# Performance work log

Hardware: AMD Instinct MI355X
Metric: run time of the kernel (lower is better)

The kernel has to match this reference:

```python
import jax, jax.numpy as jnp
import numpy as np

# --- constants matching DILConfig ---
N_DIFF = 1000      # num_diffusion_steps
STEPS = 4          # inference_steps
S_MAX = 4          # max_scales
BUDGET = 0.2       # entropy_budget
G0 = 2.0           # guidance_strength
ENT_LO = 0.1       # stability_threshold_low
ENT_HI = 0.5       # stability_threshold_high
B, L, C, H = 16, 1024, 128, 512


def setup_inputs() -> dict:
    key = jax.random.key(0)
    ks = jax.random.split(key, 6)
    y_obs = jax.random.normal(ks[0], (B, L, C), dtype=jnp.float32)
    mask = (jax.random.uniform(ks[1], (B, L, C)) > 0.5).astype(jnp.float32)
    z_init = jax.random.normal(ks[2], (B, L, C), dtype=jnp.float32)
    W1 = jax.random.normal(ks[3], (C, H), dtype=jnp.float32) / np.sqrt(C)
    b1 = jnp.zeros((H,), dtype=jnp.float32)
    W2 = jax.random.normal(ks[4], (H, C), dtype=jnp.float32) / np.sqrt(H)
    b2 = jnp.zeros((C,), dtype=jnp.float32)
    tw = jax.random.normal(ks[5], (H,), dtype=jnp.float32)
    return {"y_obs": y_obs, "mask": mask, "z_init": z_init,
            "W1": W1, "b1": b1, "W2": W2, "b2": b2, "tw": tw}


def _dil_forward(y_obs, mask, z_init, W1, b1, W2, b2, tw):
    # diffusion schedule (linear betas)
    betas = jnp.linspace(1e-4, 0.02, N_DIFF, dtype=jnp.float32)
    ac = jnp.cumprod(1.0 - betas)
    alpha = jnp.sqrt(ac)                     # sqrt_alphas_cumprod
    sigma = jnp.sqrt(1.0 - ac)               # sqrt_one_minus_alphas_cumprod
    lam = jnp.log(alpha) - jnp.log(sigma)    # log-SNR/2

    step = N_DIFF // STEPS
    ks = [N_DIFF - 1 - i * step for i in range(STEPS)]

    def score(z, k):
        # epsilon predictor: channel MLP with scalar time feature
        t_feat = jnp.float32(k) / N_DIFF
        h = jax.nn.gelu(jnp.einsum('blc,ch->blh', z, W1) + b1 + t_feat * tw)
        return jnp.einsum('blh,hc->blc', h, W2) + b2

    z = z_init
    for k in ks:  # fixed small unrolled loop over inference steps
        kp = max(k - step, 0)
        eps = score(z, k)                                   # [B,L,C]
        h_lam = lam[kp] - lam[k]
        base_a = alpha[kp] / alpha[k]
        base_b = sigma[kp] * (jnp.exp(h_lam) - 1.0)

        # entropy map: batch-mean |eps| per pixel
        ent_pix = jnp.mean(jnp.abs(eps), axis=0)            # [L,C]

        # self-guidance on observed entries
        obs_err = (z - y_obs) * mask
        guidance = -obs_err / (jnp.var(obs_err) + 1e-8)     # [B,L,C]

        z_new = z
        # coarse -> fine so finer-scale selected nodes overwrite coarser ones
        for s in range(S_MAX - 1, -1, -1):
            w = 2 ** s
            pooled = ent_pix.reshape(L // w, w, C // w, w).mean(axis=(1, 3))
            Knodes = max(1, int(BUDGET * pooled.size))
            _, idx = jax.lax.top_k(pooled.ravel(), Knodes)
            selg = jnp.zeros((pooled.size,), jnp.float32).at[idx].set(1.0)
            selg = selg.reshape(pooled.shape)
            sel = jnp.repeat(jnp.repeat(selg, w, axis=0), w, axis=1)     # [L,C]
            ent_up = jnp.repeat(jnp.repeat(pooled, w, axis=0), w, axis=1)

            # adaptive solver order from entropy stability thresholds
            order = (1.0 + (ent_up > ENT_LO).astype(jnp.float32)
                         + (ent_up > ENT_HI).astype(jnp.float32))
            corr = (1.0 + (order - 1.0) * 0.5 * h_lam
                        + (order - 1.0) * (order - 2.0) / 6.0 * h_lam ** 2)
            gs = G0 * ent_up / (ent_up + 1.0)               # adaptive guidance

            cand = base_a * z - base_b * (corr * eps) + gs * guidance
            z_new = jnp.where(sel[None, :, :] > 0, cand, z_new)
        z = z_new
    return z


def reference(y_obs, mask, z_init, W1, b1, W2, b2, tw):
    return _dil_forward(y_obs, mask, z_init, W1, b1, W2, b2, tw)
```

## Files before the change

kernel.cpp:

```cpp
#include <hip/hip_runtime.h>
#include <math.h>
#include <stdint.h>

#define L_DIM 1024
#define C_DIM 128
#define H_DIM 512
#define B_DIM 16
#define LC (L_DIM * C_DIM)
#define BLC (B_DIM * LC)

typedef __attribute__((ext_vector_type(8))) short short8;
typedef __attribute__((ext_vector_type(4))) float floatx4;

__device__ __forceinline__ unsigned fordbits(unsigned u) {
    return (u & 0x80000000u) ? ~u : (u | 0x80000000u);
}

__device__ __forceinline__ void split3(float x, unsigned& uh, unsigned& um,
                                       unsigned& ul) {
    uh = __float_as_uint(x);
    const float r1 = x - __uint_as_float(uh & 0xffff0000u);
    um = __float_as_uint(r1);
    const float r2 = r1 - __uint_as_float(um & 0xffff0000u);
    ul = __float_as_uint(r2);
}

__device__ __forceinline__ float gelu_fast(float x) {
    const float g = 0.7978845608028654f * (x + 0.044715f * x * x * x);
    const float e = __expf(2.0f * g);
    const float t = 1.0f - 2.0f / (e + 1.0f);
    return 0.5f * x * (1.0f + t);
}

__global__ __launch_bounds__(256) void wsplit_kernel(
    const float* __restrict__ W1, const float* __restrict__ W2,
    unsigned short* __restrict__ W1h, unsigned short* __restrict__ W1m,
    unsigned short* __restrict__ W1l, unsigned short* __restrict__ W2h,
    unsigned short* __restrict__ W2m, unsigned short* __restrict__ W2l,
    unsigned* __restrict__ zeroblk) {
    const int t = blockIdx.x * 256 + threadIdx.x;
    if (t < 16396) zeroblk[t] = 0u;
    unsigned uh, um, ul;
    if (t < 65536) {
        const int j = t & 7, lane = (t >> 3) & 63, nt = (t >> 9) & 31,
                  kt = (t >> 14) & 3;
        const int k = kt * 32 + (lane >> 4) * 8 + j;
        const int n = nt * 16 + (lane & 15);
        split3(W1[k * 512 + n], uh, um, ul);
        W1h[t] = (unsigned short)(uh >> 16);
        W1m[t] = (unsigned short)(um >> 16);
        W1l[t] = (unsigned short)(ul >> 16);
    } else {
        const int t2 = t - 65536;
        const int j = t2 & 7, lane = (t2 >> 3) & 63, nt = (t2 >> 9) & 7,
                  kt = (t2 >> 12) & 15;
        const int k = kt * 32 + (lane >> 4) * 8 + j;
        const int n = nt * 16 + (lane & 15);
        split3(W2[k * 128 + n], uh, um, ul);
        W2h[t2] = (unsigned short)(uh >> 16);
        W2m[t2] = (unsigned short)(um >> 16);
        W2l[t2] = (unsigned short)(ul >> 16);
    }
}

#define MFMA6(AH, AM, AL, BH, BM, BL, ACC)                                    \
    ACC = __builtin_amdgcn_mfma_f32_16x16x32_bf16(AL, BH, ACC, 0, 0, 0);      \
    ACC = __builtin_amdgcn_mfma_f32_16x16x32_bf16(AM, BM, ACC, 0, 0, 0);      \
    ACC = __builtin_amdgcn_mfma_f32_16x16x32_bf16(AH, BL, ACC, 0, 0, 0);      \
    ACC = __builtin_amdgcn_mfma_f32_16x16x32_bf16(AM, BH, ACC, 0, 0, 0);      \
    ACC = __builtin_amdgcn_mfma_f32_16x16x32_bf16(AH, BM, ACC, 0, 0, 0);      \
    ACC = __builtin_amdgcn_mfma_f32_16x16x32_bf16(AH, BH, ACC, 0, 0, 0);

__device__ __forceinline__ int swz(int row, int col) {
    return row * 128 + ((((col >> 3) ^ (row & 15))) << 3) + (col & 7);
}

template <int UPD>
__global__ __launch_bounds__(512, 2) void mlp_kernel(
    float* __restrict__ z, const float* __restrict__ zr,
    const float* __restrict__ y, const float* __restrict__ mk,
    const unsigned short* __restrict__ W1h, const unsigned short* __restrict__ W1m,
    const unsigned short* __restrict__ W1l, const unsigned short* __restrict__ W2h,
    const unsigned short* __restrict__ W2m, const unsigned short* __restrict__ W2l,
    const float* __restrict__ b1, const float* __restrict__ tw,
    const float* __restrict__ b2, float t_feat,
    float* __restrict__ eps_buf, float* __restrict__ ent,
    const float* __restrict__ cA, const float* __restrict__ cB,
    const float* __restrict__ cG, float* __restrict__ accum) {
    __shared__ unsigned short zA[3][8192];
    __shared__ unsigned short hA[3][8192];
    __shared__ float red1[8], red2[8];
    const int tid = threadIdx.x;
    const int w = tid >> 6, lane = tid & 63;
    const int quad = lane >> 4, m16 = lane & 15;
    const int l0 = blockIdx.x * 4;

    float s1 = 0.f, s2 = 0.f;
#pragma unroll
    for (int e = 0; e < 4; ++e) {
        const int f = (e * 512 + tid) * 4;
        const int r_ = f >> 7, cb = f & 127;
        const int b = r_ & 15, il = r_ >> 4, l = l0 + il;
        const size_t g = ((size_t)b * 1024 + l) * 128 + cb;
        float4 zv = *(const float4*)(zr + g);
        const float4 yv = *(const float4*)(y + g);
        const float4 mv = *(const float4*)(mk + g);
        if (UPD) {
            const float4 ev = *(const float4*)(eps_buf + g);
            const int pix = l * 128 + cb;
            const float4 a4 = *(const float4*)(cA + pix);
            const float4 b4 = *(const float4*)(cB + pix);
            const float4 g4 = *(const float4*)(cG + pix);
            zv.x = a4.x * zv.x - b4.x * ev.x - g4.x * ((zv.x - yv.x) * mv.x);
            zv.y = a4.y * zv.y - b4.y * ev.y - g4.y * ((zv.y - yv.y) * mv.y);
            zv.z = a4.z * zv.z - b4.z * ev.z - g4.z * ((zv.z - yv.z) * mv.z);
            zv.w = a4.w * zv.w - b4.w * ev.w - g4.w * ((zv.w - yv.w) * mv.w);
            *(float4*)(z + g) = zv;
        }
        float oe;
        oe = (zv.x - yv.x) * mv.x; s1 += oe; s2 += oe * oe;
        oe = (zv.y - yv.y) * mv.y; s1 += oe; s2 += oe * oe;
        oe = (zv.z - yv.z) * mv.z; s1 += oe; s2 += oe * oe;
        oe = (zv.w - yv.w) * mv.w; s1 += oe; s2 += oe * oe;

        const int base = swz(r_, cb);
        const float xs[4] = {zv.x, zv.y, zv.z, zv.w};
        ushort4 vh, vm, vl;
        unsigned uh, um, ul;
        split3(xs[0], uh, um, ul); vh.x = uh >> 16; vm.x = um >> 16; vl.x = ul >> 16;
        split3(xs[1], uh, um, ul); vh.y = uh >> 16; vm.y = um >> 16; vl.y = ul >> 16;
        split3(xs[2], uh, um, ul); vh.z = uh >> 16; vm.z = um >> 16; vl.z = ul >> 16;
        split3(xs[3], uh, um, ul); vh.w = uh >> 16; vm.w = um >> 16; vl.w = ul >> 16;
        *(ushort4*)(&zA[0][base]) = vh;
        *(ushort4*)(&zA[1][base]) = vm;
        *(ushort4*)(&zA[2][base]) = vl;
    }
#pragma unroll
    for (int off = 32; off; off >>= 1) {
        s1 += __shfl_down(s1, off);
        s2 += __shfl_down(s2, off);
    }
    if (lane == 0) { red1[w] = s1; red2[w] = s2; }
    __syncthreads();
    if (tid == 0) {
        float a1 = 0.f, a2 = 0.f;
#pragma unroll
        for (int i = 0; i < 8; ++i) { a1 += red1[i]; a2 += red2[i]; }
        atomicAdd(&accum[0], a1);
        atomicAdd(&accum[1], a2);
    }

    floatx4 acc1[16];
#pragma unroll
    for (int i = 0; i < 16; ++i) acc1[i] = (floatx4){0.f, 0.f, 0.f, 0.f};

#pragma unroll
    for (int kt = 0; kt < 4; ++kt) {
        short8 Ah[4], Am[4], Al[4];
#pragma unroll
        for (int il = 0; il < 4; ++il) {
            const int fb = swz(il * 16 + m16, kt * 32 + quad * 8);
            Ah[il] = *(const short8*)(&zA[0][fb]);
            Am[il] = *(const short8*)(&zA[1][fb]);
            Al[il] = *(const short8*)(&zA[2][fb]);
        }
#pragma unroll
        for (int q = 0; q < 4; ++q) {
            const size_t off = ((size_t)(kt * 32 + q * 8 + w) * 64 + lane) * 8;
            const short8 bh = *(const short8*)(W1h + off);
            const short8 bm = *(const short8*)(W1m + off);
            const short8 bl = *(const short8*)(W1l + off);
#pragma unroll
            for (int il = 0; il < 4; ++il) {
                floatx4 a = acc1[q * 4 + il];
                MFMA6(Ah[il], Am[il], Al[il], bh, bm, bl, a);
                acc1[q * 4 + il] = a;
            }
        }
    }

    floatx4 acc2[4];
#pragma unroll
    for (int i = 0; i < 4; ++i) acc2[i] = (floatx4){0.f, 0.f, 0.f, 0.f};

#pragma unroll
    for (int q = 0; q < 4; ++q) {
        {
            const int colg = q * 128 + w * 16 + m16;
            const float bb = b1[colg] + t_feat * tw[colg];
            const int kcol = w * 16 + m16;
#pragma unroll
            for (int il = 0; il < 4; ++il) {
#pragma unroll
                for (int r = 0; r < 4; ++r) {
                    const float x = gelu_fast(acc1[q * 4 + il][r] + bb);
                    unsigned uh, um, ul;
                    split3(x, uh, um, ul);
                    const int idx = swz(il * 16 + quad * 4 + r, kcol);
                    hA[0][idx] = (unsigned short)(uh >> 16);
                    hA[1][idx] = (unsigned short)(um >> 16);
                    hA[2][idx] = (unsigned short)(ul >> 16);
                }
            }
        }
        __syncthreads();

#pragma unroll
        for (int ktl = 0; ktl < 4; ++ktl) {
            short8 Ah2[4], Am2[4], Al2[4];
#pragma unroll
            for (int il = 0; il < 4; ++il) {
                const int fb = swz(il * 16 + m16, ktl * 32 + quad * 8);
                Ah2[il] = *(const short8*)(&hA[0][fb]);
                Am2[il] = *(const short8*)(&hA[1][fb]);
                Al2[il] = *(const short8*)(&hA[2][fb]);
            }
            const size_t off =
                ((size_t)((q * 4 + ktl) * 8 + w) * 64 + lane) * 8;
            const short8 bh = *(const short8*)(W2h + off);
            const short8 bm = *(const short8*)(W2m + off);
            const short8 bl = *(const short8*)(W2l + off);
#pragma unroll
            for (int il = 0; il < 4; ++il) {
                floatx4 a = acc2[il];
                MFMA6(Ah2[il], Am2[il], Al2[il], bh, bm, bl, a);
                acc2[il] = a;
            }
        }
        __syncthreads();
    }

    {
        const int col = w * 16 + m16;
        const float bb2 = b2[col];
#pragma unroll
        for (int il = 0; il < 4; ++il) {
            float pa = 0.f;
#pragma unroll
            for (int r = 0; r < 4; ++r) {
                const float e = acc2[il][r] + bb2;
                const int b = quad * 4 + r;
                eps_buf[((size_t)b * 1024 + l0 + il) * 128 + col] = e;
                pa += fabsf(e);
            }
            pa += __shfl_xor(pa, 16);
            pa += __shfl_xor(pa, 32);
            if (quad == 0) ent[(l0 + il) * 128 + col] = pa * (1.0f / 16.0f);
        }
    }
}


__global__ __launch_bounds__(256) void pools_kernel(
    const float* __restrict__ ent, float* __restrict__ p1,
    float* __restrict__ p2, float* __restrict__ p3,
    unsigned* __restrict__ ghist) {
    __shared__ unsigned lh[8192];
    const int tid = threadIdx.x;
    const int gid = blockIdx.x * 256 + tid;
    for (int i = tid; i < 8192; i += 256) lh[i] = 0u;
    __syncthreads();

    {
        const float2 ev = *(const float2*)(ent + (size_t)gid * 2);
        const unsigned b0 = fordbits(__float_as_uint(ev.x)) >> 18;
        const unsigned b1_ = fordbits(__float_as_uint(ev.y)) >> 18;
        atomicAdd(&lh[b0 >> 1], 1u << ((b0 & 1) << 4));
        atomicAdd(&lh[b1_ >> 1], 1u << ((b1_ & 1) << 4));
    }
    if (gid < 32768) {
        const int r = gid >> 6, c = gid & 63;
        float s = 0.f;
#pragma unroll
        for (int ii = 0; ii < 2; ++ii) {
            const float2 e = *(const float2*)(ent + (((r * 2 + ii) << 7) + c * 2));
            s += e.x; s += e.y;
        }
        p1[gid] = s * 0.25f;
    }
    if (gid < 8192) {
        const int r = gid >> 5, c = gid & 31;
        float s = 0.f;
#pragma unroll
        for (int ii = 0; ii < 4; ++ii) {
            const float4 e = *(const float4*)(ent + (((r * 4 + ii) << 7) + c * 4));
            s += e.x; s += e.y; s += e.z; s += e.w;
        }
        p2[gid] = s * 0.0625f;
    }
    if (gid < 2048) {
        const int r = gid >> 4, c = gid & 15;
        float s = 0.f;
#pragma unroll
        for (int ii = 0; ii < 8; ++ii) {
            const float4 ea = *(const float4*)(ent + (((r * 8 + ii) << 7) + c * 8));
            const float4 eb = *(const float4*)(ent + (((r * 8 + ii) << 7) + c * 8 + 4));
            s += ea.x; s += ea.y; s += ea.z; s += ea.w;
            s += eb.x; s += eb.y; s += eb.z; s += eb.w;
        }
        p3[gid] = s * (1.0f / 64.0f);
    }
    __syncthreads();
    for (int i = tid; i < 8192; i += 256) {
        const unsigned v = lh[i];
        if (v & 0xFFFFu) atomicAdd(&ghist[2 * i], v & 0xFFFFu);
        if (v >> 16) atomicAdd(&ghist[2 * i + 1], v >> 16);
    }
}

#define CAND_CAP 16384

template <int NPT4, int N, unsigned K>
__device__ __forceinline__ void small_select(
    const float* __restrict__ data, unsigned* __restrict__ gout, const int t,
    const int w8, unsigned* __restrict__ histcand,
    unsigned* __restrict__ part, unsigned (*hrep)[512],
    unsigned* sh_b, unsigned* sh_krem, unsigned* sh_cnt, unsigned* sh_d,
    unsigned* sh_k2) {
    float4 xv[NPT4];
#pragma unroll
    for (int i = 0; i < NPT4; ++i) {
        const int idx4 = t + i * 1024;
        if (idx4 < (N >> 2)) xv[i] = ((const float4*)data)[idx4];
        else xv[i] = (float4){-1e30f, -1e30f, -1e30f, -1e30f};
    }
    unsigned u[NPT4 * 4];
#pragma unroll
    for (int i = 0; i < NPT4; ++i) {
        u[4 * i + 0] = fordbits(__float_as_uint(xv[i].x));
        u[4 * i + 1] = fordbits(__float_as_uint(xv[i].y));
        u[4 * i + 2] = fordbits(__float_as_uint(xv[i].z));
        u[4 * i + 3] = fordbits(__float_as_uint(xv[i].w));
    }
    if (t == 0) { *sh_b = 0u; *sh_krem = 1u; *sh_cnt = 0u; *sh_d = 0u; *sh_k2 = 1u; }
    for (int i = t; i < 16384; i += 1024) histcand[i] = 0u;
    __syncthreads();
#pragma unroll
    for (int j = 0; j < NPT4 * 4; ++j) atomicAdd(&histcand[u[j] >> 18], 1u);
    __syncthreads();
    {
        unsigned s = 0;
#pragma unroll
        for (int j = 0; j < 16; ++j) s += histcand[t * 16 + j];
        part[t] = s;
    }
    __syncthreads();
    for (int off = 1; off < 1024; off <<= 1) {
        const unsigned v = (t + off < 1024) ? part[t + off] : 0u;
        __syncthreads();
        part[t] += v;
        __syncthreads();
    }
    {
        const unsigned suf = part[t];
        const unsigned sufn = (t < 1023) ? part[t + 1] : 0u;
        if (suf >= K && sufn < K) {
            unsigned run = sufn;
            for (int b = 15; b >= 0; --b) {
                const unsigned hb = histcand[t * 16 + b];
                run += hb;
                if (run >= K) {
                    *sh_b = (unsigned)(t * 16 + b);
                    *sh_krem = K - (run - hb);
                    break;
                }
            }
        }
    }
    __syncthreads();
    const unsigned b14 = *sh_b;
    unsigned krem = *sh_krem;
    __syncthreads();
#pragma unroll
    for (int j = 0; j < NPT4 * 4; ++j)
        if ((u[j] >> 18) == b14) {
            const unsigned p = atomicAdd(sh_cnt, 1u);
            if (p < CAND_CAP) histcand[p] = u[j];
        }
    __syncthreads();
    const unsigned cnt = *sh_cnt;
    const bool inlds = (cnt <= CAND_CAP);
    for (int i = t; i < 4096; i += 1024) ((unsigned*)hrep)[i] = 0u;
    __syncthreads();
    if (inlds) {
        for (unsigned i = t; i < cnt; i += 1024)
            atomicAdd(&hrep[w8][(histcand[i] >> 9) & 511u], 1u);
    } else {
#pragma unroll
        for (int j = 0; j < NPT4 * 4; ++j)
            if ((u[j] >> 18) == b14)
                atomicAdd(&hrep[w8][(u[j] >> 9) & 511u], 1u);
    }
    __syncthreads();
    if (t < 512) {
        unsigned s = 0;
#pragma unroll
        for (int r = 0; r < 8; ++r) s += hrep[r][t];
        part[t] = s;
    }
    __syncthreads();
    for (int off = 1; off < 512; off <<= 1) {
        unsigned v = 0u;
        if (t < 512) v = (t + off < 512) ? part[t + off] : 0u;
        __syncthreads();
        if (t < 512) part[t] += v;
        __syncthreads();
    }
    if (t < 512) {
        const unsigned suf = part[t];
        const unsigned sufn = (t < 511) ? part[t + 1] : 0u;
        if (suf >= krem && sufn < krem) { *sh_d = (unsigned)t; *sh_k2 = krem - sufn; }
    }
    __syncthreads();
    const unsigned dA = *sh_d;
    krem = *sh_k2;
    __syncthreads();
    for (int i = t; i < 4096; i += 1024) ((unsigned*)hrep)[i] = 0u;
    __syncthreads();
    if (inlds) {
        for (unsigned i = t; i < cnt; i += 1024) {
            const unsigned c = histcand[i];
            if (((c >> 9) & 511u) == dA) atomicAdd(&hrep[w8][c & 511u], 1u);
        }
    } else {
#pragma unroll
        for (int j = 0; j < NPT4 * 4; ++j)
            if ((u[j] >> 18) == b14 && ((u[j] >> 9) & 511u) == dA)
                atomicAdd(&hrep[w8][u[j] & 511u], 1u);
    }
    __syncthreads();
    if (t < 512) {
        unsigned s = 0;
#pragma unroll
        for (int r = 0; r < 8; ++r) s += hrep[r][t];
        part[t] = s;
    }
    __syncthreads();
    for (int off = 1; off < 512; off <<= 1) {
        unsigned v = 0u;
        if (t < 512) v = (t + off < 512) ? part[t + off] : 0u;
        __syncthreads();
        if (t < 512) part[t] += v;
        __syncthreads();
    }
    if (t < 512) {
        const unsigned suf = part[t];
        const unsigned sufn = (t < 511) ? part[t + 1] : 0u;
        if (suf >= krem && sufn < krem)
            gout[0] = (b14 << 18) | (dA << 9) | (unsigned)t;
    }
}

__global__ __launch_bounds__(1024, 1) void thresh_kernel(
    const float* __restrict__ ent, const float* __restrict__ p1,
    const float* __restrict__ p2, const float* __restrict__ p3,
    const unsigned* __restrict__ ghist, unsigned* __restrict__ gprefix) {
    const int scale = blockIdx.x, t = threadIdx.x;
    __shared__ unsigned histcand[16384];
    __shared__ unsigned part[1024];
    __shared__ unsigned hrep[8][512];
    __shared__ unsigned sh_b, sh_krem, sh_cnt, sh_d, sh_k2;
    const int w8 = (t >> 6) & 7;

    if (scale == 1) {
        small_select<8, 32768, 6553u>(p1, &gprefix[1], t, w8, histcand, part,
                                      hrep, &sh_b, &sh_krem, &sh_cnt, &sh_d,
                                      &sh_k2);
        return;
    }
    if (scale == 2) {
        small_select<2, 8192, 1638u>(p2, &gprefix[2], t, w8, histcand, part,
                                     hrep, &sh_b, &sh_krem, &sh_cnt, &sh_d,
                                     &sh_k2);
        return;
    }
    if (scale == 3) {
        small_select<1, 2048, 409u>(p3, &gprefix[3], t, w8, histcand, part,
                                    hrep, &sh_b, &sh_krem, &sh_cnt, &sh_d,
                                    &sh_k2);
        return;
    }

    const unsigned K = 26214u;
    if (t == 0) { sh_b = 0u; sh_krem = 1u; sh_cnt = 0u; sh_d = 0u; sh_k2 = 1u; }

    {
        unsigned s = 0;
        const uint4* h4 = (const uint4*)(ghist + t * 16);
#pragma unroll
        for (int j = 0; j < 4; ++j) {
            const uint4 x = h4[j];
            s += x.x + x.y + x.z + x.w;
        }
        part[t] = s;
    }
    __syncthreads();
    for (int off = 1; off < 1024; off <<= 1) {
        const unsigned v = (t + off < 1024) ? part[t + off] : 0u;
        __syncthreads();
        part[t] += v;
        __syncthreads();
    }
    {
        const unsigned suf = part[t];
        const unsigned sufn = (t < 1023) ? part[t + 1] : 0u;
        if (suf >= K && sufn < K) {
            unsigned run = sufn;
            for (int b = 15; b >= 0; --b) {
                const unsigned hb = ghist[t * 16 + b];
                run += hb;
                if (run >= K) {
                    sh_b = (unsigned)(t * 16 + b);
                    sh_krem = K - (run - hb);
                    break;
                }
            }
        }
    }
    __syncthreads();
    const unsigned b14 = sh_b;
    unsigned krem = sh_krem;

    for (int base = 0; base < 32768; base += 8192) {
        float4 w4[8];
#pragma unroll
        for (int i = 0; i < 8; ++i)
            w4[i] = ((const float4*)ent)[base + i * 1024 + t];
#pragma unroll
        for (int i = 0; i < 8; ++i) {
            const float xs[4] = {w4[i].x, w4[i].y, w4[i].z, w4[i].w};
#pragma unroll
            for (int j = 0; j < 4; ++j) {
                const unsigned uu = fordbits(__float_as_uint(xs[j]));
                if ((uu >> 18) == b14) {
                    const unsigned p = atomicAdd(&sh_cnt, 1u);
                    if (p < CAND_CAP) histcand[p] = uu;
                }
            }
        }
    }
    __syncthreads();
    const unsigned cnt = sh_cnt;
    const bool inlds = (cnt <= CAND_CAP);

    for (int i = t; i < 4096; i += 1024) ((unsigned*)hrep)[i] = 0u;
    __syncthreads();
    if (inlds) {
        for (unsigned i = t; i < cnt; i += 1024)
            atomicAdd(&hrep[w8][(histcand[i] >> 9) & 511u], 1u);
    } else {
        for (int base = 0; base < 32768; base += 8192) {
            float4 w4[8];
#pragma unroll
            for (int i = 0; i < 8; ++i)
                w4[i] = ((const float4*)ent)[base + i * 1024 + t];
#pragma unroll
            for (int i = 0; i < 8; ++i) {
                const float xs[4] = {w4[i].x, w4[i].y, w4[i].z, w4[i].w};
#pragma unroll
                for (int j = 0; j < 4; ++j) {
                    const unsigned uu = fordbits(__float_as_uint(xs[j]));
                    if ((uu >> 18) == b14)
                        atomicAdd(&hrep[w8][(uu >> 9) & 511u], 1u);
                }
            }
        }
    }
    __syncthreads();
    if (t < 512) {
        unsigned s = 0;
#pragma unroll
        for (int r = 0; r < 8; ++r) s += hrep[r][t];
        part[t] = s;
    }
    __syncthreads();
    for (int off = 1; off < 512; off <<= 1) {
        unsigned v = 0u;
        if (t < 512) v = (t + off < 512) ? part[t + off] : 0u;
        __syncthreads();
        if (t < 512) part[t] += v;
        __syncthreads();
    }
    if (t < 512) {
        const unsigned suf = part[t];
        const unsigned sufn = (t < 511) ? part[t + 1] : 0u;
        if (suf >= krem && sufn < krem) { sh_d = (unsigned)t; sh_k2 = krem - sufn; }
    }
    __syncthreads();
    const unsigned dA = sh_d;
    krem = sh_k2;
    __syncthreads();

    for (int i = t; i < 4096; i += 1024) ((unsigned*)hrep)[i] = 0u;
    __syncthreads();
    if (inlds) {
        for (unsigned i = t; i < cnt; i += 1024) {
            const unsigned c = histcand[i];
            if (((c >> 9) & 511u) == dA) atomicAdd(&hrep[w8][c & 511u], 1u);
        }
    } else {
        for (int base = 0; base < 32768; base += 8192) {
            float4 w4[8];
#pragma unroll
            for (int i = 0; i < 8; ++i)
                w4[i] = ((const float4*)ent)[base + i * 1024 + t];
#pragma unroll
            for (int i = 0; i < 8; ++i) {
                const float xs[4] = {w4[i].x, w4[i].y, w4[i].z, w4[i].w};
#pragma unroll
                for (int j = 0; j < 4; ++j) {
                    const unsigned uu = fordbits(__float_as_uint(xs[j]));
                    if ((uu >> 18) == b14 && ((uu >> 9) & 511u) == dA)
                        atomicAdd(&hrep[w8][uu & 511u], 1u);
                }
            }
        }
    }
    __syncthreads();
    if (t < 512) {
        unsigned s = 0;
#pragma unroll
        for (int r = 0; r < 8; ++r) s += hrep[r][t];
        part[t] = s;
    }
    __syncthreads();
    for (int off = 1; off < 512; off <<= 1) {
        unsigned v = 0u;
        if (t < 512) v = (t + off < 512) ? part[t + off] : 0u;
        __syncthreads();
        if (t < 512) part[t] += v;
        __syncthreads();
    }
    if (t < 512) {
        const unsigned suf = part[t];
        const unsigned sufn = (t < 511) ? part[t + 1] : 0u;
        if (suf >= krem && sufn < krem)
            gprefix[0] = (b14 << 18) | (dA << 9) | (unsigned)t;
    }
}

__global__ __launch_bounds__(256) void coeff_kernel(
    const float* __restrict__ ent, const float* __restrict__ p1,
    const float* __restrict__ p2, const float* __restrict__ p3,
    const unsigned* __restrict__ gprefix, const float* __restrict__ accum_si,
    float* __restrict__ cA, float* __restrict__ cB, float* __restrict__ cG,
    unsigned* __restrict__ ghist, float base_a, float base_b, float h_lam) {
    const int i = blockIdx.x * 256 + threadIdx.x;
    if (i < 16384) ghist[i] = 0u;

    const unsigned t0 = gprefix[0], t1 = gprefix[1], t2 = gprefix[2],
                   t3 = gprefix[3];
    const float mean = accum_si[0] * (1.0f / (float)BLC);
    const float var = accum_si[1] * (1.0f / (float)BLC) - mean * mean;
    const float vinv = 1.0f / (var + 1e-8f);

    const int l = i >> 7, c = i & 127;
    float ent_v = 0.f;
    bool sel = false;
    const float v0 = ent[i];
    if (fordbits(__float_as_uint(v0)) >= t0) { ent_v = v0; sel = true; }
    else {
        const float v1 = p1[((l >> 1) << 6) + (c >> 1)];
        if (fordbits(__float_as_uint(v1)) >= t1) { ent_v = v1; sel = true; }
        else {
            const float v2 = p2[((l >> 2) << 5) + (c >> 2)];
            if (fordbits(__float_as_uint(v2)) >= t2) { ent_v = v2; sel = true; }
            else {
                const float v3 = p3[((l >> 3) << 4) + (c >> 3)];
                if (fordbits(__float_as_uint(v3)) >= t3) { ent_v = v3; sel = true; }
            }
        }
    }
    if (sel) {
        float corr;
        if (ent_v > 0.5f)
            corr = 1.0f + h_lam + h_lam * h_lam * (1.0f / 3.0f);
        else if (ent_v > 0.1f)
            corr = 1.0f + 0.5f * h_lam;
        else
            corr = 1.0f;
        cA[i] = base_a;
        cB[i] = base_b * corr;
        cG[i] = (2.0f * ent_v / (ent_v + 1.0f)) * vinv;
    } else {
        cA[i] = 1.0f;
        cB[i] = 0.f;
        cG[i] = 0.f;
    }
}

__global__ __launch_bounds__(256) void update_kernel(
    float* __restrict__ z, const float* __restrict__ y,
    const float* __restrict__ mk, const float* __restrict__ eps,
    const float* __restrict__ cA, const float* __restrict__ cB,
    const float* __restrict__ cG) {
    const int idx = blockIdx.x * 256 + threadIdx.x;
    const int p = idx & (LC - 1);
    const float zi = z[idx];
    z[idx] = cA[p] * zi - cB[p] * eps[idx] - cG[p] * ((zi - y[idx]) * mk[idx]);
}

extern "C" void kernel_launch(void* const* d_in, const int* in_sizes, int n_in,
                              void* d_out, int out_size, void* d_ws,
                              size_t ws_size, hipStream_t stream) {
    const float* y_obs = (const float*)d_in[0];
    const float* mask = (const float*)d_in[1];
    const float* z_init = (const float*)d_in[2];
    const float* W1 = (const float*)d_in[3];
    const float* b1 = (const float*)d_in[4];
    const float* W2 = (const float*)d_in[5];
    const float* b2 = (const float*)d_in[6];
    const float* tw = (const float*)d_in[7];
    float* z = (float*)d_out;
    float* ws = (float*)d_ws;

    float* eps = ws;
    float* ent = ws + 2097152;
    float* p1 = ws + 2228224;
    float* p2 = ws + 2260992;
    float* p3 = ws + 2269184;
    float* cA = ws + 2271232;
    float* cB = ws + 2402304;
    float* cG = ws + 2533376;
    float* accum = ws + 2664448;
    unsigned* gprefix = (unsigned*)(ws + 2664456);
    unsigned* ghist = (unsigned*)(ws + 2664460);
    unsigned short* W1h = (unsigned short*)(ws + 2680844);
    unsigned short* W1m = (unsigned short*)(ws + 2713612);
    unsigned short* W1l = (unsigned short*)(ws + 2746380);
    unsigned short* W2h = (unsigned short*)(ws + 2779148);
    unsigned short* W2m = (unsigned short*)(ws + 2811916);
    unsigned short* W2l = (unsigned short*)(ws + 2844684);

    float alpha_[1000], sigma_[1000], lam_[1000];
    {
        float ac = 1.0f;
        for (int i = 0; i < 1000; ++i) {
            const float beta = 1e-4f + (0.02f - 1e-4f) * ((float)i / 999.0f);
            ac = ac * (1.0f - beta);
            alpha_[i] = sqrtf(ac);
            sigma_[i] = sqrtf(1.0f - ac);
            lam_[i] = logf(alpha_[i]) - logf(sigma_[i]);
        }
    }
    float tf[4], hl[4], ba[4], bb[4];
    for (int si = 0; si < 4; ++si) {
        const int k = 999 - si * 250;
        const int kp = (k - 250 > 0) ? (k - 250) : 0;
        tf[si] = (float)k / 1000.0f;
        hl[si] = lam_[kp] - lam_[k];
        ba[si] = alpha_[kp] / alpha_[k];
        bb[si] = sigma_[kp] * (expf(hl[si]) - 1.0f);
    }

    wsplit_kernel<<<512, 256, 0, stream>>>(W1, W2, W1h, W1m, W1l, W2h, W2m,
                                           W2l, (unsigned*)accum);

    for (int si = 0; si < 4; ++si) {
        const float* zrd = (si <= 1) ? z_init : z;
        if (si == 0) {
            mlp_kernel<0><<<256, 512, 0, stream>>>(
                z, zrd, y_obs, mask, W1h, W1m, W1l, W2h, W2m, W2l, b1, tw, b2,
                tf[0], eps, ent, cA, cB, cG, accum);
        } else {
            mlp_kernel<1><<<256, 512, 0, stream>>>(
                z, zrd, y_obs, mask, W1h, W1m, W1l, W2h, W2m, W2l, b1, tw, b2,
                tf[si], eps, ent, cA, cB, cG, accum + 2 * si);
        }
        pools_kernel<<<256, 256, 0, stream>>>(ent, p1, p2, p3, ghist);
        thresh_kernel<<<4, 1024, 0, stream>>>(ent, p1, p2, p3, ghist, gprefix);
        coeff_kernel<<<512, 256, 0, stream>>>(ent, p1, p2, p3, gprefix,
                                              accum + 2 * si, cA, cB, cG,
                                              ghist, ba[si], bb[si], hl[si]);
    }
    update_kernel<<<8192, 256, 0, stream>>>(z, y_obs, mask, eps, cA, cB, cG);
}
```

Before: 384.2 us.

## Fuse entropy pooling and histogram into MLP kernel and prefetch weight fragments

Removes the separate pools_kernel by computing the 2x2 and 4x4 pooled entropy and the global radix histogram inside the MLP kernel's epilogue, reusing the hA shared buffer for the local histogram. The 8x8 pooling moves into the scale-3 block of thresh_kernel. It also software-pipelines the W1/W2 bf16 fragment loads by prefetching the next fragment before the current MFMAs. This saves one launch per step and a re-read of the entropy map, at the cost of more registers and a longer serial tail in the MLP kernel.

Result: faster. 370.5 us (median of 2 runs) (-3.6%).

```diff
diff --git a/kernel.cpp b/kernel.cpp
--- a/kernel.cpp
+++ b/kernel.cpp
@@ -86,9 +86,12 @@
     const float* __restrict__ b2, float t_feat,
     float* __restrict__ eps_buf, float* __restrict__ ent,
     const float* __restrict__ cA, const float* __restrict__ cB,
-    const float* __restrict__ cG, float* __restrict__ accum) {
+    const float* __restrict__ cG, float* __restrict__ accum,
+    float* __restrict__ p1, float* __restrict__ p2,
+    unsigned* __restrict__ ghist) {
     __shared__ unsigned short zA[3][8192];
     __shared__ unsigned short hA[3][8192];
+    __shared__ float entbuf[4][128];
     __shared__ float red1[8], red2[8];
     const int tid = threadIdx.x;
     const int w = tid >> 6, lane = tid & 63;
@@ -154,28 +157,43 @@
 #pragma unroll
     for (int i = 0; i < 16; ++i) acc1[i] = (floatx4){0.f, 0.f, 0.f, 0.f};
 
-#pragma unroll
-    for (int kt = 0; kt < 4; ++kt) {
+    {
         short8 Ah[4], Am[4], Al[4];
-#pragma unroll
-        for (int il = 0; il < 4; ++il) {
-            const int fb = swz(il * 16 + m16, kt * 32 + quad * 8);
-            Ah[il] = *(const short8*)(&zA[0][fb]);
-            Am[il] = *(const short8*)(&zA[1][fb]);
-            Al[il] = *(const short8*)(&zA[2][fb]);
-        }
-#pragma unroll
-        for (int q = 0; q < 4; ++q) {
-            const size_t off = ((size_t)(kt * 32 + q * 8 + w) * 64 + lane) * 8;
-            const short8 bh = *(const short8*)(W1h + off);
-            const short8 bm = *(const short8*)(W1m + off);
-            const short8 bl = *(const short8*)(W1l + off);
+        short8 bh, bm, bl;
+        {
+            const size_t off0 = ((size_t)w * 64 + lane) * 8;
+            bh = *(const short8*)(W1h + off0);
+            bm = *(const short8*)(W1m + off0);
+            bl = *(const short8*)(W1l + off0);
+        }
+#pragma unroll
+        for (int it = 0; it < 16; ++it) {
+            const int kt = it >> 2, q = it & 3;
+            if (q == 0) {
+#pragma unroll
+                for (int il = 0; il < 4; ++il) {
+                    const int fb = swz(il * 16 + m16, kt * 32 + quad * 8);
+                    Ah[il] = *(const short8*)(&zA[0][fb]);
+                    Am[il] = *(const short8*)(&zA[1][fb]);
+                    Al[il] = *(const short8*)(&zA[2][fb]);
+                }
+            }
+            short8 nbh = bh, nbm = bm, nbl = bl;
+            if (it < 15) {
+                const int itn = it + 1;
+                const size_t off =
+                    ((size_t)((itn >> 2) * 32 + (itn & 3) * 8 + w) * 64 + lane) * 8;
+                nbh = *(const short8*)(W1h + off);
+                nbm = *(const short8*)(W1m + off);
+                nbl = *(const short8*)(W1l + off);
+            }
 #pragma unroll
             for (int il = 0; il < 4; ++il) {
                 floatx4 a = acc1[q * 4 + il];
                 MFMA6(Ah[il], Am[il], Al[il], bh, bm, bl, a);
                 acc1[q * 4 + il] = a;
             }
+            bh = nbh; bm = nbm; bl = nbl;
         }
     }
 
@@ -183,6 +201,13 @@
 #pragma unroll
     for (int i = 0; i < 4; ++i) acc2[i] = (floatx4){0.f, 0.f, 0.f, 0.f};
 
+    short8 ch, cm, cl;
+    {
+        const size_t off0 = ((size_t)w * 64 + lane) * 8;
+        ch = *(const short8*)(W2h + off0);
+        cm = *(const short8*)(W2m + off0);
+        cl = *(const short8*)(W2l + off0);
+    }
 #pragma unroll
     for (int q = 0; q < 4; ++q) {
         {
@@ -207,6 +232,14 @@
 
 #pragma unroll
         for (int ktl = 0; ktl < 4; ++ktl) {
+            const int jt = q * 4 + ktl;
+            short8 nch = ch, ncm = cm, ncl = cl;
+            if (jt < 15) {
+                const size_t off = ((size_t)((jt + 1) * 8 + w) * 64 + lane) * 8;
+                nch = *(const short8*)(W2h + off);
+                ncm = *(const short8*)(W2m + off);
+                ncl = *(const short8*)(W2l + off);
+            }
             short8 Ah2[4], Am2[4], Al2[4];
 #pragma unroll
             for (int il = 0; il < 4; ++il) {
@@ -215,17 +248,13 @@
                 Am2[il] = *(const short8*)(&hA[1][fb]);
                 Al2[il] = *(const short8*)(&hA[2][fb]);
             }
-            const size_t off =
-                ((size_t)((q * 4 + ktl) * 8 + w) * 64 + lane) * 8;
-            const short8 bh = *(const short8*)(W2h + off);
-            const short8 bm = *(const short8*)(W2m + off);
-            const short8 bl = *(const short8*)(W2l + off);
 #pragma unroll
             for (int il = 0; il < 4; ++il) {
                 floatx4 a = acc2[il];
-                MFMA6(Ah2[il], Am2[il], Al2[il], bh, bm, bl, a);
+                MFMA6(Ah2[il], Am2[il], Al2[il], ch, cm, cl, a);
                 acc2[il] = a;
             }
+            ch = nch; cm = ncm; cl = ncl;
         }
         __syncthreads();
     }
@@ -245,85 +274,60 @@
             }
             pa += __shfl_xor(pa, 16);
             pa += __shfl_xor(pa, 32);
-            if (quad == 0) ent[(l0 + il) * 128 + col] = pa * (1.0f / 16.0f);
-        }
-    }
-}
-
-
-__global__ __launch_bounds__(256) void pools_kernel(
-    const float* __restrict__ ent, float* __restrict__ p1,
-    float* __restrict__ p2, float* __restrict__ p3,
-    unsigned* __restrict__ ghist) {
-    __shared__ unsigned lh[8192];
-    const int tid = threadIdx.x;
-    const int gid = blockIdx.x * 256 + tid;
-    for (int i = tid; i < 8192; i += 256) lh[i] = 0u;
-    __syncthreads();
-
-    {
-        const float2 ev = *(const float2*)(ent + (size_t)gid * 2);
-        const unsigned b0 = fordbits(__float_as_uint(ev.x)) >> 18;
-        const unsigned b1_ = fordbits(__float_as_uint(ev.y)) >> 18;
-        atomicAdd(&lh[b0 >> 1], 1u << ((b0 & 1) << 4));
-        atomicAdd(&lh[b1_ >> 1], 1u << ((b1_ & 1) << 4));
-    }
-    if (gid < 32768) {
-        const int r = gid >> 6, c = gid & 63;
+            if (quad == 0) {
+                const float ev = pa * (1.0f / 16.0f);
+                ent[(l0 + il) * 128 + col] = ev;
+                entbuf[il][col] = ev;
+            }
+        }
+    }
+
+    unsigned* lhist = (unsigned*)&hA[0][0];
+    for (int i = tid; i < 8192; i += 512) lhist[i] = 0u;
+    __syncthreads();
+    if (tid < 512) {
+        const float v = entbuf[tid >> 7][tid & 127];
+        const unsigned b = fordbits(__float_as_uint(v)) >> 18;
+        atomicAdd(&lhist[b >> 1], 1u << ((b & 1) << 4));
+    }
+    if (tid < 128) {
+        const int ir = tid >> 6, c = tid & 63;
+        float s = entbuf[2 * ir][2 * c];
+        s += entbuf[2 * ir][2 * c + 1];
+        s += entbuf[2 * ir + 1][2 * c];
+        s += entbuf[2 * ir + 1][2 * c + 1];
+        p1[(2 * (int)blockIdx.x + ir) * 64 + c] = s * 0.25f;
+    }
+    if (tid < 32) {
+        const int c = tid;
         float s = 0.f;
 #pragma unroll
-        for (int ii = 0; ii < 2; ++ii) {
-            const float2 e = *(const float2*)(ent + (((r * 2 + ii) << 7) + c * 2));
-            s += e.x; s += e.y;
-        }
-        p1[gid] = s * 0.25f;
-    }
-    if (gid < 8192) {
-        const int r = gid >> 5, c = gid & 31;
-        float s = 0.f;
-#pragma unroll
         for (int ii = 0; ii < 4; ++ii) {
-            const float4 e = *(const float4*)(ent + (((r * 4 + ii) << 7) + c * 4));
-            s += e.x; s += e.y; s += e.z; s += e.w;
-        }
-        p2[gid] = s * 0.0625f;
-    }
-    if (gid < 2048) {
-        const int r = gid >> 4, c = gid & 15;
-        float s = 0.f;
-#pragma unroll
-        for (int ii = 0; ii < 8; ++ii) {
-            const float4 ea = *(const float4*)(ent + (((r * 8 + ii) << 7) + c * 8));
-            const float4 eb = *(const float4*)(ent + (((r * 8 + ii) << 7) + c * 8 + 4));
-            s += ea.x; s += ea.y; s += ea.z; s += ea.w;
-            s += eb.x; s += eb.y; s += eb.z; s += eb.w;
-        }
-        p3[gid] = s * (1.0f / 64.0f);
-    }
-    __syncthreads();
-    for (int i = tid; i < 8192; i += 256) {
-        const unsigned v = lh[i];
+            s += entbuf[ii][4 * c];
+            s += entbuf[ii][4 * c + 1];
+            s += entbuf[ii][4 * c + 2];
+            s += entbuf[ii][4 * c + 3];
+        }
+        p2[(int)blockIdx.x * 32 + c] = s * 0.0625f;
+    }
+    __syncthreads();
+    for (int i = tid; i < 8192; i += 512) {
+        const unsigned v = lhist[i];
         if (v & 0xFFFFu) atomicAdd(&ghist[2 * i], v & 0xFFFFu);
         if (v >> 16) atomicAdd(&ghist[2 * i + 1], v >> 16);
     }
 }
 
+
 #define CAND_CAP 16384
 
 template <int NPT4, int N, unsigned K>
-__device__ __forceinline__ void small_select(
-    const float* __restrict__ data, unsigned* __restrict__ gout, const int t,
+__device__ __forceinline__ void small_select_vals(
+    const float4* xv, unsigned* __restrict__ gout, const int t,
     const int w8, unsigned* __restrict__ histcand,
     unsigned* __restrict__ part, unsigned (*hrep)[512],
     unsigned* sh_b, unsigned* sh_krem, unsigned* sh_cnt, unsigned* sh_d,
     unsigned* sh_k2) {
-    float4 xv[NPT4];
-#pragma unroll
-    for (int i = 0; i < NPT4; ++i) {
-        const int idx4 = t + i * 1024;
-        if (idx4 < (N >> 2)) xv[i] = ((const float4*)data)[idx4];
-        else xv[i] = (float4){-1e30f, -1e30f, -1e30f, -1e30f};
-    }
     unsigned u[NPT4 * 4];
 #pragma unroll
     for (int i = 0; i < NPT4; ++i) {
@@ -453,7 +457,7 @@
 
 __global__ __launch_bounds__(1024, 1) void thresh_kernel(
     const float* __restrict__ ent, const float* __restrict__ p1,
-    const float* __restrict__ p2, const float* __restrict__ p3,
+    const float* __restrict__ p2, float* __restrict__ p3,
     const unsigned* __restrict__ ghist, unsigned* __restrict__ gprefix) {
     const int scale = blockIdx.x, t = threadIdx.x;
     __shared__ unsigned histcand[16384];
@@ -463,21 +467,51 @@
     const int w8 = (t >> 6) & 7;
 
     if (scale == 1) {
-        small_select<8, 32768, 6553u>(p1, &gprefix[1], t, w8, histcand, part,
-                                      hrep, &sh_b, &sh_krem, &sh_cnt, &sh_d,
-                                      &sh_k2);
+        float4 xv[8];
+#pragma unroll
+        for (int i = 0; i < 8; ++i) xv[i] = ((const float4*)p1)[t + i * 1024];
+        small_select_vals<8, 32768, 6553u>(xv, &gprefix[1], t, w8, histcand,
+                                           part, hrep, &sh_b, &sh_krem,
+                                           &sh_cnt, &sh_d, &sh_k2);
         return;
     }
     if (scale == 2) {
-        small_select<2, 8192, 1638u>(p2, &gprefix[2], t, w8, histcand, part,
-                                     hrep, &sh_b, &sh_krem, &sh_cnt, &sh_d,
-                                     &sh_k2);
+        float4 xv[2];
+#pragma unroll
+        for (int i = 0; i < 2; ++i) xv[i] = ((const float4*)p2)[t + i * 1024];
+        small_select_vals<2, 8192, 1638u>(xv, &gprefix[2], t, w8, histcand,
+                                          part, hrep, &sh_b, &sh_krem,
+                                          &sh_cnt, &sh_d, &sh_k2);
         return;
     }
     if (scale == 3) {
-        small_select<1, 2048, 409u>(p3, &gprefix[3], t, w8, histcand, part,
-                                    hrep, &sh_b, &sh_krem, &sh_cnt, &sh_d,
-                                    &sh_k2);
+        float4 xv[1];
+        if (t < 512) {
+            float sv[4];
+#pragma unroll
+            for (int jdx = 0; jdx < 4; ++jdx) {
+                const int e = t * 4 + jdx;
+                const int r = e >> 4, c = e & 15;
+                float s = 0.f;
+#pragma unroll
+                for (int ii = 0; ii < 8; ++ii) {
+                    const float4 ea =
+                        *(const float4*)(ent + (((r * 8 + ii) << 7) + c * 8));
+                    const float4 eb =
+                        *(const float4*)(ent + (((r * 8 + ii) << 7) + c * 8 + 4));
+                    s += ea.x; s += ea.y; s += ea.z; s += ea.w;
+                    s += eb.x; s += eb.y; s += eb.z; s += eb.w;
+                }
+                sv[jdx] = s * (1.0f / 64.0f);
+            }
+            xv[0] = (float4){sv[0], sv[1], sv[2], sv[3]};
+            *(float4*)(p3 + t * 4) = xv[0];
+        } else {
+            xv[0] = (float4){-1e30f, -1e30f, -1e30f, -1e30f};
+        }
+        small_select_vals<1, 2048, 409u>(xv, &gprefix[3], t, w8, histcand,
+                                         part, hrep, &sh_b, &sh_krem,
+                                         &sh_cnt, &sh_d, &sh_k2);
         return;
     }
 
@@ -761,13 +795,12 @@
         if (si == 0) {
             mlp_kernel<0><<<256, 512, 0, stream>>>(
                 z, zrd, y_obs, mask, W1h, W1m, W1l, W2h, W2m, W2l, b1, tw, b2,
-                tf[0], eps, ent, cA, cB, cG, accum);
+                tf[0], eps, ent, cA, cB, cG, accum, p1, p2, ghist);
         } else {
             mlp_kernel<1><<<256, 512, 0, stream>>>(
                 z, zrd, y_obs, mask, W1h, W1m, W1l, W2h, W2m, W2l, b1, tw, b2,
-                tf[si], eps, ent, cA, cB, cG, accum + 2 * si);
-        }
-        pools_kernel<<<256, 256, 0, stream>>>(ent, p1, p2, p3, ghist);
+                tf[si], eps, ent, cA, cB, cG, accum + 2 * si, p1, p2, ghist);
+        }
         thresh_kernel<<<4, 1024, 0, stream>>>(ent, p1, p2, p3, ghist, gprefix);
         coeff_kernel<<<512, 256, 0, stream>>>(ent, p1, p2, p3, gprefix,
                                               accum + 2 * si, cA, cB, cG,
```
